# Optimization experiments

Hardware: AMD Instinct MI355X
Metric: run time of the kernel (lower is better)

The kernel has to match this reference:

```python
import jax, jax.numpy as jnp
import numpy as np

# ---- constants matching init_kwargs ----
N_GRID = 512
DX = 1.0 / N_GRID
INV_DX = float(N_GRID)
DT = 1e-4
P_VOL = (DX * 0.5) ** 2
P_RHO = 1.0
P_MASS = P_VOL * P_RHO
GRAVITY = 10.0
N_PART = 2_000_000


def setup_inputs() -> dict:
    key = jax.random.key(0)
    k = jax.random.split(key, 5)
    # positions safely inside the domain so the 3x3 stencil never leaves the grid
    x = 0.1 + 0.8 * jax.random.uniform(k[0], (N_PART, 2), dtype=jnp.float32)
    v = 0.1 * jax.random.normal(k[1], (N_PART, 2), dtype=jnp.float32)
    C = 0.5 * jax.random.normal(k[2], (N_PART, 2, 2), dtype=jnp.float32)
    # deformation gradient near identity -> det(F) > 0 (physical MPM state)
    F = jnp.eye(2, dtype=jnp.float32)[None] + 0.01 * jax.random.normal(k[3], (N_PART, 2, 2), dtype=jnp.float32)
    material = jax.random.randint(k[4], (N_PART,), 0, 3, dtype=jnp.int32)
    Jp = jnp.ones((N_PART,), dtype=jnp.float32)
    E = jnp.array([1000.0], dtype=jnp.float32)
    nu = jnp.array([0.2], dtype=jnp.float32)
    return {"x": x, "v": v, "C": C, "F": F, "material": material, "Jp": Jp, "E": E, "nu": nu}


def _quad_weights(fx):
    # quadratic B-spline weights; fx: (N,2), returns list of 3 arrays (N,2)
    return [0.5 * (1.5 - fx) ** 2, 0.75 - (fx - 1.0) ** 2, 0.5 * (fx - 0.5) ** 2]


def _polar_rotation_and_J(F):
    # Closed-form 2x2 polar decomposition F = R S. For det(F) > 0 this R equals
    # U @ Vh from the (embedded 3x3) SVD used by the torch code, and
    # J = prod(singular values) = |det F|.
    a = F[:, 0, 0] + F[:, 1, 1]
    b = F[:, 1, 0] - F[:, 0, 1]
    r = jnp.sqrt(a * a + b * b)
    c, s = a / r, b / r
    R = jnp.stack([jnp.stack([c, -s], -1), jnp.stack([s, c], -1)], -2)  # (N,2,2)
    J = jnp.abs(F[:, 0, 0] * F[:, 1, 1] - F[:, 0, 1] * F[:, 1, 0])
    return R, J


def _step(x, v, C, F, Jp, E, nu):
    mu0 = E / (2.0 * (1.0 + nu))                      # (1,)
    la0 = E * nu / ((1.0 + nu) * (1.0 - 2.0 * nu))    # (1,)

    base = (x * INV_DX - 0.5).astype(jnp.int32)       # (N,2)
    fx = x * INV_DX - base.astype(jnp.float32)        # (N,2)
    w = _quad_weights(fx)

    # deformation gradient update: F <- F + dt * C @ F
    F = F + DT * jnp.einsum('nij,njk->nik', C, F)

    h = jnp.exp(10.0 * (1.0 - Jp))                    # (N,)
    mu, la = mu0 * h, la0 * h                         # (N,)

    R, J = _polar_rotation_and_J(F)
    # 2*mu*(F - R) @ F^T + I * lambda*J*(J-1)
    PF = jnp.einsum('nij,nkj->nik', F - R, F)
    I2 = jnp.eye(2, dtype=F.dtype)
    stress = 2.0 * mu[:, None, None] * PF + I2[None] * (la * J * (J - 1.0))[:, None, None]
    stress = (-DT * P_VOL * 4.0 * INV_DX ** 2) * stress
    affine = stress + P_MASS * C                      # (N,2,2)

    # ---- P2G scatter: grid_v += w * (m*v + affine @ dpos), grid_m += w*m ----
    # (identical to the torch trick of scattering m*v - affine@x and affine,
    #  then adding scatter(affine) @ grid_x, since grid_x - x = (offset - fx)*dx)
    ncell = N_GRID * N_GRID
    grid_v = jnp.zeros((ncell, 2), dtype=F.dtype)
    grid_m = jnp.zeros((ncell,), dtype=F.dtype)
    mv = P_MASS * v
    for i in range(3):
        for j in range(3):
            off = jnp.array([i, j], dtype=fx.dtype)
            weight = w[i][:, 0] * w[j][:, 1]                      # (N,)
            dpos = (off - fx) * DX                                # (N,2)
            contrib = weight[:, None] * (mv + jnp.einsum('nij,nj->ni', affine, dpos))
            idx = (base[:, 0] + i) * N_GRID + (base[:, 1] + j)    # (N,)
            grid_v = grid_v.at[idx].add(contrib)
            grid_m = grid_m.at[idx].add(weight * P_MASS)
    grid_v = grid_v.reshape(N_GRID, N_GRID, 2)
    grid_m = grid_m.reshape(N_GRID, N_GRID)

    # momentum -> velocity only where mass > 0
    nonempty = grid_m > 0
    grid_v = jnp.where(nonempty[..., None], grid_v / jnp.maximum(grid_m, 1e-30)[..., None], grid_v)
    grid_v = grid_v.at[:, :, 1].add(-DT * GRAVITY)
    # boundary conditions
    grid_v = grid_v.at[:3, :, 0].set(jnp.maximum(grid_v[:3, :, 0], 0.0))
    grid_v = grid_v.at[-2:, :, 0].set(jnp.minimum(grid_v[-2:, :, 0], 0.0))
    grid_v = grid_v.at[:, :3, 1].set(jnp.maximum(grid_v[:, :3, 1], 0.0))
    grid_v = grid_v.at[:, -2:, 1].set(jnp.minimum(grid_v[:, -2:, 1], 0.0))

    # ---- G2P gather ----
    gv_flat = grid_v.reshape(ncell, 2)
    new_v = jnp.zeros_like(v)
    new_C = jnp.zeros_like(C)
    for i in range(3):
        for j in range(3):
            off = jnp.array([i, j], dtype=fx.dtype)
            weight = w[i][:, 0] * w[j][:, 1]
            dpos = (off - fx) * DX
            idx = (base[:, 0] + i) * N_GRID + (base[:, 1] + j)
            gv = gv_flat[idx]                                      # (N,2)
            new_v = new_v + weight[:, None] * gv
            new_C = new_C + (4.0 * INV_DX ** 2) * weight[:, None, None] * gv[:, :, None] * dpos[:, None, :]

    x = x + DT * new_v
    return x, new_v, new_C, F


def reference(x, v, C, F, material, Jp, E, nu):
    xn, vn, Cn, Fn = _step(x, v, C, F, Jp, E, nu)
    return (xn, vn, Cn, Fn, material, Jp)
```

## Files before the change

### kernel.cpp

```cpp
#include <hip/hip_runtime.h>

namespace {
constexpr int   NGRID  = 512;
constexpr int   NCELL  = NGRID * NGRID;
constexpr float DX     = 1.0f / (float)NGRID;
constexpr float INV_DX = (float)NGRID;
constexpr float DT     = 1e-4f;
constexpr float P_VOL  = (DX * 0.5f) * (DX * 0.5f);
constexpr float P_MASS = P_VOL * 1.0f;
constexpr float GRAV   = 10.0f;

constexpr int TILE  = 16;
constexpr int TPR   = NGRID / TILE;
constexpr int NTILE = TPR * TPR;
constexpr int REG   = TILE + 3;
constexpr int RCELL = REG * REG;
constexpr int NBLK  = 512;
constexpr int BLK   = 256;
constexpr int PBLK  = 512;
constexpr int CAP   = 3456;
constexpr int BINS  = 17 * 17;
}


__device__ __forceinline__ float quadw(int d, float fx) {
    const float t0 = 1.5f - fx, t1 = fx - 1.0f, t2 = fx - 0.5f;
    const float w0 = 0.5f * t0 * t0;
    const float w1 = 0.75f - t1 * t1;
    const float w2 = 0.5f * t2 * t2;
    return d == 0 ? w0 : (d == 1 ? w1 : w2);
}

__global__ __launch_bounds__(256) void k_count(
    const float2* __restrict__ x, int n, int ppb,
    int* __restrict__ cnt )
{
    __shared__ int hist[NTILE];
    for (int t = threadIdx.x; t < NTILE; t += BLK) hist[t] = 0;
    __syncthreads();
    const int b0 = blockIdx.x * ppb;
    const int b1 = min(b0 + ppb, n);
    for (int p = b0 + threadIdx.x; p < b1; p += BLK) {
        const float2 xp = x[p];
        const int ci = (int)(xp.x * INV_DX);
        const int cj = (int)(xp.y * INV_DX);
        atomicAdd(&hist[(ci >> 4) * TPR + (cj >> 4)], 1);
    }
    __syncthreads();
    int* row = cnt + (size_t)blockIdx.x * NTILE;
    for (int t = threadIdx.x; t < NTILE; t += BLK) row[t] = hist[t];
}

__global__ __launch_bounds__(1024) void k_scan(
    int* __restrict__ cnt, int* __restrict__ tile_start, int* __restrict__ tile_end)
{
    const int t = threadIdx.x;
    int s = 0;
    #pragma unroll 8
    for (int b = 0; b < NBLK; ++b) s += cnt[(size_t)b * NTILE + t];

    __shared__ int wsum[16];
    const int lane = t & 63, w = t >> 6;
    int inc = s;
    #pragma unroll
    for (int d = 1; d < 64; d <<= 1) {
        int u = __shfl_up(inc, d, 64);
        if (lane >= d) inc += u;
    }
    if (lane == 63) wsum[w] = inc;
    __syncthreads();
    if (t == 0) {
        int r = 0;
        #pragma unroll
        for (int i = 0; i < 16; ++i) { int v = wsum[i]; wsum[i] = r; r += v; }
    }
    __syncthreads();
    const int base = wsum[w] + inc - s;
    tile_start[t] = base;
    tile_end[t]   = base + s;

    int run = base;
    #pragma unroll 8
    for (int b = 0; b < NBLK; ++b) {
        int v = cnt[(size_t)b * NTILE + t];
        cnt[(size_t)b * NTILE + t] = run;
        run += v;
    }
}

__global__ __launch_bounds__(256) void k_scatter(
    const float2* __restrict__ x,
    const float2* __restrict__ v,
    const float4* __restrict__ C,
    const float4* __restrict__ F,
    const int*    __restrict__ material,
    const float*  __restrict__ Jp,
    const float*  __restrict__ Ep,
    const float*  __restrict__ nup,
    int n, int ppb,
    const int* __restrict__ cnt,
    float4* __restrict__ packed,
    float4* __restrict__ outF,
    float*  __restrict__ outMat,
    float*  __restrict__ outJp)
{
    __shared__ int cur[NTILE];
    {
        const int* row = cnt + (size_t)blockIdx.x * NTILE;
        for (int t = threadIdx.x; t < NTILE; t += BLK) cur[t] = row[t];
    }
    __syncthreads();

    const float E  = Ep[0];
    const float nu = nup[0];
    const float mu0 = E / (2.0f * (1.0f + nu));
    const float la0 = E * nu / ((1.0f + nu) * (1.0f - 2.0f * nu));

    const int b0 = blockIdx.x * ppb;
    const int b1 = min(b0 + ppb, n);
    for (int p = b0 + threadIdx.x; p < b1; p += BLK) {
        const float2 xp = x[p];
        const float2 vp = v[p];
        const float4 c4 = C[p];
        const float4 f4 = F[p];
        const float  jp = Jp[p];

        const float F00 = f4.x + DT * (c4.x * f4.x + c4.y * f4.z);
        const float F01 = f4.y + DT * (c4.x * f4.y + c4.y * f4.w);
        const float F10 = f4.z + DT * (c4.z * f4.x + c4.w * f4.z);
        const float F11 = f4.w + DT * (c4.z * f4.y + c4.w * f4.w);

        const float h  = expf(10.0f * (1.0f - jp));
        const float mu = mu0 * h;
        const float la = la0 * h;

        const float a = F00 + F11;
        const float b = F10 - F01;
        const float r = sqrtf(a * a + b * b);
        const float cth = a / r;
        const float sth = b / r;
        const float J = fabsf(F00 * F11 - F01 * F10);

        const float A00 = F00 - cth, A01 = F01 + sth;
        const float A10 = F10 - sth, A11 = F11 - cth;
        const float PF00 = A00 * F00 + A01 * F01;
        const float PF01 = A00 * F10 + A01 * F11;
        const float PF10 = A10 * F00 + A11 * F01;
        const float PF11 = A10 * F10 + A11 * F11;

        constexpr float SC = -DT * P_VOL * 4.0f * INV_DX * INV_DX;
        const float diag = la * J * (J - 1.0f);
        const float twomu = 2.0f * mu;
        const float Af00 = SC * (twomu * PF00 + diag) + P_MASS * c4.x;
        const float Af01 = SC * (twomu * PF01)        + P_MASS * c4.y;
        const float Af10 = SC * (twomu * PF10)        + P_MASS * c4.z;
        const float Af11 = SC * (twomu * PF11 + diag) + P_MASS * c4.w;

        const int ci = (int)(xp.x * INV_DX);
        const int cj = (int)(xp.y * INV_DX);
        const int t  = (ci >> 4) * TPR + (cj >> 4);
        const int slot = atomicAdd(&cur[t], 1);

        packed[2 * (size_t)slot]     = make_float4(xp.x, xp.y, P_MASS * vp.x, P_MASS * vp.y);
        packed[2 * (size_t)slot + 1] = make_float4(Af00, Af01, Af10, Af11);

        outF[p]   = make_float4(F00, F01, F10, F11);
        outMat[p] = (float)material[p];
        outJp[p]  = jp;
    }
}

__global__ __launch_bounds__(PBLK) void k_p2g_tile(
    const float4* __restrict__ packed,
    const int* __restrict__ tile_start,
    const int* __restrict__ tile_end,
    float* __restrict__ gvx, float* __restrict__ gvy, float* __restrict__ gm)
{
    const int t  = blockIdx.x;
    const int s0 = tile_start[t];
    const int s1 = tile_end[t];
    if (s0 == s1) return;

    __shared__ float4 rec[2 * CAP];
    __shared__ unsigned short perm[CAP];
    __shared__ unsigned short binof[CAP];
    __shared__ int bcnt[BINS];
    __shared__ int boffs[BINS];
    __shared__ int wscan[8];

    const int tid = threadIdx.x;
    const int tr = t >> 5, tc = t & 31;
    const int r0 = tr * TILE - 1, c0 = tc * TILE - 1;

    const int nseg = s1 - s0;
    const int nin  = min(nseg, CAP);
    const bool ovf = (nseg > CAP);

    for (int b = tid; b < BINS; b += PBLK) bcnt[b] = 0;
    __syncthreads();

    for (int k = tid; k < nin; k += PBLK) {
        const float4 pa = packed[2 * (size_t)(s0 + k)];
        const float4 pb = packed[2 * (size_t)(s0 + k) + 1];
        rec[2 * k]     = pa;
        rec[2 * k + 1] = pb;
        const int bi = (int)(pa.x * INV_DX - 0.5f);
        const int bj = (int)(pa.y * INV_DX - 0.5f);
        const int bin = (bi - r0) * 17 + (bj - c0);
        binof[k] = (unsigned short)bin;
        atomicAdd(&bcnt[bin], 1);
    }
    __syncthreads();

    int vv = 0, incl = 0;
    if (tid < 320) {
        vv = (tid < BINS) ? bcnt[tid] : 0;
        incl = vv;
        const int lane = tid & 63;
        #pragma unroll
        for (int d = 1; d < 64; d <<= 1) {
            int u = __shfl_up(incl, d, 64);
            if (lane >= d) incl += u;
        }
        if (lane == 63) wscan[tid >> 6] = incl;
    }
    __syncthreads();
    if (tid == 0) {
        int run = 0;
        #pragma unroll
        for (int i = 0; i < 5; ++i) { int w = wscan[i]; wscan[i] = run; run += w; }
    }
    __syncthreads();
    if (tid < BINS) {
        const int excl = incl - vv + wscan[tid >> 6];
        boffs[tid] = excl;
        bcnt[tid]  = excl;
    }
    __syncthreads();

    for (int k = tid; k < nin; k += PBLK) {
        const int bin = binof[k];
        const int rk = atomicAdd(&bcnt[bin], 1);
        perm[rk] = (unsigned short)k;
    }
    __syncthreads();

    if (ovf) {
        for (int k = CAP + tid; k < nseg; k += PBLK) {
            const float4 pa = packed[2 * (size_t)(s0 + k)];
            const float4 pb = packed[2 * (size_t)(s0 + k) + 1];
            const float xs = pa.x * INV_DX, ys = pa.y * INV_DX;
            const int bi = (int)(xs - 0.5f), bj = (int)(ys - 0.5f);
            const float fxx = xs - (float)bi, fxy = ys - (float)bj;
            for (int i = 0; i < 3; ++i)
                for (int j = 0; j < 3; ++j) {
                    const float wgt = quadw(i, fxx) * quadw(j, fxy);
                    const float dpx = ((float)i - fxx) * DX;
                    const float dpy = ((float)j - fxy) * DX;
                    const int g = (bi + i) * NGRID + (bj + j);
                    atomicAdd(&gvx[g], wgt * (pa.z + pb.x * dpx + pb.y * dpy));
                    atomicAdd(&gvy[g], wgt * (pa.w + pb.z * dpx + pb.w * dpy));
                    atomicAdd(&gm[g],  wgt * P_MASS);
                }
        }
    }

    for (int idx = tid; idx < RCELL; idx += PBLK) {
        const int lr = idx / REG, lc = idx % REG;
        float vx = 0.0f, vy = 0.0f, m = 0.0f;

        #pragma unroll
        for (int di = 0; di < 3; ++di) {
            const int bli = lr - di;
            if ((unsigned)bli > 16u) continue;
            #pragma unroll
            for (int dj = 0; dj < 3; ++dj) {
                const int blj = lc - dj;
                if ((unsigned)blj > 16u) continue;
                const int b = bli * 17 + blj;
                const int k0 = boffs[b], k1 = bcnt[b];
                for (int k = k0; k < k1; ++k) {
                    const int pp = perm[k];
                    const float4 pa = rec[2 * pp];
                    const float4 pb = rec[2 * pp + 1];
                    const float xs = pa.x * INV_DX, ys = pa.y * INV_DX;
                    const float fxx = xs - (float)((int)(xs - 0.5f));
                    const float fxy = ys - (float)((int)(ys - 0.5f));
                    const float wgt = quadw(di, fxx) * quadw(dj, fxy);
                    const float dpx = ((float)di - fxx) * DX;
                    const float dpy = ((float)dj - fxy) * DX;
                    vx += wgt * (pa.z + pb.x * dpx + pb.y * dpy);
                    vy += wgt * (pa.w + pb.z * dpx + pb.w * dpy);
                    m  += wgt * P_MASS;
                }
            }
        }

        const int gr = r0 + lr, gc = c0 + lc;
        if ((unsigned)gr >= (unsigned)NGRID || (unsigned)gc >= (unsigned)NGRID) continue;
        const int g = gr * NGRID + gc;
        const bool interior = (lr >= 3 && lr <= 15 && lc >= 3 && lc <= 15) && !ovf;
        if (interior) {
            gvx[g] = vx; gvy[g] = vy; gm[g] = m;
        } else {
            if (vx != 0.0f) atomicAdd(&gvx[g], vx);
            if (vy != 0.0f) atomicAdd(&gvy[g], vy);
            if (m  != 0.0f) atomicAdd(&gm[g],  m);
        }
    }
}

__global__ __launch_bounds__(256) void k_grid(
    const float* __restrict__ gvx, const float* __restrict__ gvy,
    const float* __restrict__ gm, float2* __restrict__ gv)
{
    const int idx = blockIdx.x * blockDim.x + threadIdx.x;
    if (idx >= NCELL) return;
    const int i = idx >> 9;
    const int j = idx & (NGRID - 1);
    float m = gm[idx], vx = gvx[idx], vy = gvy[idx];
    if (m > 0.0f) {
        const float inv = 1.0f / fmaxf(m, 1e-30f);
        vx *= inv; vy *= inv;
    }
    vy -= DT * GRAV;
    if (i < 3)          vx = fmaxf(vx, 0.0f);
    if (i >= NGRID - 2) vx = fminf(vx, 0.0f);
    if (j < 3)          vy = fmaxf(vy, 0.0f);
    if (j >= NGRID - 2) vy = fminf(vy, 0.0f);
    gv[idx] = make_float2(vx, vy);
}

__global__ __launch_bounds__(256) void k_g2p(
    const float2* __restrict__ x,
    const float2* __restrict__ gv,
    float2* __restrict__ outX,
    float2* __restrict__ outV,
    float4* __restrict__ outC,
    int n)
{
    const int p = blockIdx.x * blockDim.x + threadIdx.x;
    if (p >= n) return;

    const float2 xp = x[p];
    const float xs = xp.x * INV_DX, ys = xp.y * INV_DX;
    const int bi = (int)(xs - 0.5f);
    const int bj = (int)(ys - 0.5f);
    const float fxx = xs - (float)bi;
    const float fxy = ys - (float)bj;

    float wx[3], wy[3];
    { float t0 = 1.5f - fxx, t1 = fxx - 1.0f, t2 = fxx - 0.5f;
      wx[0] = 0.5f * t0 * t0; wx[1] = 0.75f - t1 * t1; wx[2] = 0.5f * t2 * t2; }
    { float t0 = 1.5f - fxy, t1 = fxy - 1.0f, t2 = fxy - 0.5f;
      wy[0] = 0.5f * t0 * t0; wy[1] = 0.75f - t1 * t1; wy[2] = 0.5f * t2 * t2; }

    float nvx = 0.0f, nvy = 0.0f;
    float C00 = 0.0f, C01 = 0.0f, C10 = 0.0f, C11 = 0.0f;
    constexpr float K4 = 4.0f * INV_DX * INV_DX;

    #pragma unroll
    for (int i = 0; i < 3; ++i) {
        const float dpx = ((float)i - fxx) * DX;
        const int rowbase = (bi + i) * NGRID + bj;
        #pragma unroll
        for (int j = 0; j < 3; ++j) {
            const float wgt = wx[i] * wy[j];
            const float dpy = ((float)j - fxy) * DX;
            const float2 g = gv[rowbase + j];
            nvx += wgt * g.x;
            nvy += wgt * g.y;
            const float kw = K4 * wgt;
            C00 += kw * g.x * dpx;
            C01 += kw * g.x * dpy;
            C10 += kw * g.y * dpx;
            C11 += kw * g.y * dpy;
        }
    }

    outX[p] = make_float2(xp.x + DT * nvx, xp.y + DT * nvy);
    outV[p] = make_float2(nvx, nvy);
    outC[p] = make_float4(C00, C01, C10, C11);
}

__global__ __launch_bounds__(256) void fb_p2g(
    const float2* __restrict__ x, const float2* __restrict__ v,
    const float4* __restrict__ C, const float4* __restrict__ F,
    const int* __restrict__ material, const float* __restrict__ Jp,
    const float* __restrict__ Ep, const float* __restrict__ nup,
    float* __restrict__ g,
    float4* __restrict__ outF, float* __restrict__ outMat, float* __restrict__ outJp,
    int n)
{
    const int p = blockIdx.x * blockDim.x + threadIdx.x;
    if (p >= n) return;
    const float E = Ep[0], nu = nup[0];
    const float mu0 = E / (2.0f * (1.0f + nu));
    const float la0 = E * nu / ((1.0f + nu) * (1.0f - 2.0f * nu));
    const float2 xp = x[p]; const float2 vp = v[p];
    const float4 c4 = C[p]; const float4 f4 = F[p];
    const float jp = Jp[p];
    const float xs = xp.x * INV_DX, ys = xp.y * INV_DX;
    const int bi = (int)(xs - 0.5f), bj = (int)(ys - 0.5f);
    const float fxx = xs - (float)bi, fxy = ys - (float)bj;
    float wx[3], wy[3];
    { float t0 = 1.5f - fxx, t1 = fxx - 1.0f, t2 = fxx - 0.5f;
      wx[0] = 0.5f * t0 * t0; wx[1] = 0.75f - t1 * t1; wx[2] = 0.5f * t2 * t2; }
    { float t0 = 1.5f - fxy, t1 = fxy - 1.0f, t2 = fxy - 0.5f;
      wy[0] = 0.5f * t0 * t0; wy[1] = 0.75f - t1 * t1; wy[2] = 0.5f * t2 * t2; }
    const float F00 = f4.x + DT * (c4.x * f4.x + c4.y * f4.z);
    const float F01 = f4.y + DT * (c4.x * f4.y + c4.y * f4.w);
    const float F10 = f4.z + DT * (c4.z * f4.x + c4.w * f4.z);
    const float F11 = f4.w + DT * (c4.z * f4.y + c4.w * f4.w);
    const float h = expf(10.0f * (1.0f - jp));
    const float mu = mu0 * h, la = la0 * h;
    const float a = F00 + F11, b = F10 - F01;
    const float r = sqrtf(a * a + b * b);
    const float cth = a / r, sth = b / r;
    const float J = fabsf(F00 * F11 - F01 * F10);
    const float A00 = F00 - cth, A01 = F01 + sth;
    const float A10 = F10 - sth, A11 = F11 - cth;
    constexpr float SC = -DT * P_VOL * 4.0f * INV_DX * INV_DX;
    const float diag = la * J * (J - 1.0f);
    const float twomu = 2.0f * mu;
    const float Af00 = SC * (twomu * (A00 * F00 + A01 * F01) + diag) + P_MASS * c4.x;
    const float Af01 = SC * (twomu * (A00 * F10 + A01 * F11))        + P_MASS * c4.y;
    const float Af10 = SC * (twomu * (A10 * F00 + A11 * F01))        + P_MASS * c4.z;
    const float Af11 = SC * (twomu * (A10 * F10 + A11 * F11) + diag) + P_MASS * c4.w;
    const float mvx = P_MASS * vp.x, mvy = P_MASS * vp.y;
    #pragma unroll
    for (int i = 0; i < 3; ++i) {
        #pragma unroll
        for (int j = 0; j < 3; ++j) {
            const float wgt = wx[i] * wy[j];
            const float dpx = ((float)i - fxx) * DX;
            const float dpy = ((float)j - fxy) * DX;
            const size_t k3 = (size_t)((bi + i) * NGRID + (bj + j)) * 3;
            atomicAdd(&g[k3 + 0], wgt * (mvx + Af00 * dpx + Af01 * dpy));
            atomicAdd(&g[k3 + 1], wgt * (mvy + Af10 * dpx + Af11 * dpy));
            atomicAdd(&g[k3 + 2], wgt * P_MASS);
        }
    }
    outF[p] = make_float4(F00, F01, F10, F11);
    outMat[p] = (float)material[p];
    outJp[p] = jp;
}

__global__ __launch_bounds__(256) void fb_grid(
    const float* __restrict__ g, float2* __restrict__ gv)
{
    const int idx = blockIdx.x * blockDim.x + threadIdx.x;
    if (idx >= NCELL) return;
    const int i = idx >> 9, j = idx & (NGRID - 1);
    float vx = g[(size_t)idx * 3], vy = g[(size_t)idx * 3 + 1], m = g[(size_t)idx * 3 + 2];
    if (m > 0.0f) { const float inv = 1.0f / fmaxf(m, 1e-30f); vx *= inv; vy *= inv; }
    vy -= DT * GRAV;
    if (i < 3)          vx = fmaxf(vx, 0.0f);
    if (i >= NGRID - 2) vx = fminf(vx, 0.0f);
    if (j < 3)          vy = fmaxf(vy, 0.0f);
    if (j >= NGRID - 2) vy = fminf(vy, 0.0f);
    gv[idx] = make_float2(vx, vy);
}

extern "C" void kernel_launch(void* const* d_in, const int* in_sizes, int n_in,
                              void* d_out, int out_size, void* d_ws, size_t ws_size,
                              hipStream_t stream) {
    const int n = in_sizes[0] / 2;

    const float2* x   = (const float2*)d_in[0];
    const float2* v   = (const float2*)d_in[1];
    const float4* C   = (const float4*)d_in[2];
    const float4* F   = (const float4*)d_in[3];
    const int*    mat = (const int*)d_in[4];
    const float*  Jp  = (const float*)d_in[5];
    const float*  Ep  = (const float*)d_in[6];
    const float*  nup = (const float*)d_in[7];

    float* out = (float*)d_out;
    float2* o_x = (float2*)(out);
    float2* o_v = (float2*)(out + 2 * (size_t)n);
    float4* o_C = (float4*)(out + 4 * (size_t)n);
    float4* o_F = (float4*)(out + 8 * (size_t)n);
    float*  o_m = out + 12 * (size_t)n;
    float*  o_J = out + 13 * (size_t)n;

    const int BLOCK = 256;
    const int pgrid = (n + BLOCK - 1) / BLOCK;
    const int ggrid = (NCELL + BLOCK - 1) / BLOCK;

    char* w = (char*)d_ws;
    float4* packed = (float4*)w;            w += (size_t)n * 2 * sizeof(float4);
    int* cnt    = (int*)w;                  w += (size_t)NBLK * NTILE * sizeof(int);
    int* tstart = (int*)w;                  w += (size_t)NTILE * sizeof(int);
    int* tend   = (int*)w;                  w += (size_t)NTILE * sizeof(int);
    float* gvx  = (float*)w;                w += (size_t)NCELL * sizeof(float);
    float* gvy  = (float*)w;                w += (size_t)NCELL * sizeof(float);
    float* gm   = (float*)w;                w += (size_t)NCELL * sizeof(float);
    float2* gfin= (float2*)w;               w += (size_t)NCELL * sizeof(float2);
    const size_t need = (size_t)(w - (char*)d_ws);

    if (ws_size >= need) {
        const int ppb = (n + NBLK - 1) / NBLK;
        hipMemsetAsync(gvx, 0, (size_t)NCELL * 3 * sizeof(float), stream);
        k_count  <<<NBLK, BLOCK, 0, stream>>>(x, n, ppb, cnt);
        k_scan   <<<1, 1024, 0, stream>>>(cnt, tstart, tend);
        k_scatter<<<NBLK, BLOCK, 0, stream>>>(x, v, C, F, mat, Jp, Ep, nup,
                                              n, ppb, cnt, packed, o_F, o_m, o_J);
        k_p2g_tile<<<NTILE, PBLK, 0, stream>>>(packed, tstart, tend, gvx, gvy, gm);
        k_grid   <<<ggrid, BLOCK, 0, stream>>>(gvx, gvy, gm, gfin);
        k_g2p    <<<pgrid, BLOCK, 0, stream>>>(x, gfin, o_x, o_v, o_C, n);
    } else {
        float* g = (float*)d_ws;
        float2* gf = (float2*)(g + (size_t)NCELL * 3);
        hipMemsetAsync(g, 0, (size_t)NCELL * 3 * sizeof(float), stream);
        fb_p2g <<<pgrid, BLOCK, 0, stream>>>(x, v, C, F, mat, Jp, Ep, nup,
                                             g, o_F, o_m, o_J, n);
        fb_grid<<<ggrid, BLOCK, 0, stream>>>(g, gf);
        k_g2p  <<<pgrid, BLOCK, 0, stream>>>(x, gf, o_x, o_v, o_C, n);
    }
}
```

Baseline: 497.2 us.

## Drop shared particle staging in P2G tile kernel and merge bin-row loops

The tile P2G kernel no longer copies particle records into a large shared-memory buffer. It only reads positions to bin them, then the gather loop reads the packed particle data straight from global memory, relying on the cache. The three per-column bin loops are merged into one contiguous range per bin row, and the column offset is computed per particle. Block size drops from 512 to 384 threads. Freeing about 110KB of LDS should allow more blocks per CU, but every cell now issues repeated global or L2 loads in place of LDS reads.

Result: slower. 566.7 us (+14.0%).

```diff
diff --git a/kernel.cpp b/kernel.cpp
--- a/kernel.cpp
+++ b/kernel.cpp
@@ -17,7 +17,7 @@
 constexpr int RCELL = REG * REG;
 constexpr int NBLK  = 512;
 constexpr int BLK   = 256;
-constexpr int PBLK  = 512;
+constexpr int PBLK  = 384;
 constexpr int CAP   = 3456;
 constexpr int BINS  = 17 * 17;
 }
@@ -181,7 +181,6 @@
     const int s1 = tile_end[t];
     if (s0 == s1) return;
 
-    __shared__ float4 rec[2 * CAP];
     __shared__ unsigned short perm[CAP];
     __shared__ unsigned short binof[CAP];
     __shared__ int bcnt[BINS];
@@ -200,12 +199,9 @@
     __syncthreads();
 
     for (int k = tid; k < nin; k += PBLK) {
-        const float4 pa = packed[2 * (size_t)(s0 + k)];
-        const float4 pb = packed[2 * (size_t)(s0 + k) + 1];
-        rec[2 * k]     = pa;
-        rec[2 * k + 1] = pb;
-        const int bi = (int)(pa.x * INV_DX - 0.5f);
-        const int bj = (int)(pa.y * INV_DX - 0.5f);
+        const float2 xy = *(const float2*)&packed[2 * (size_t)(s0 + k)];
+        const int bi = (int)(xy.x * INV_DX - 0.5f);
+        const int bj = (int)(xy.y * INV_DX - 0.5f);
         const int bin = (bi - r0) * 17 + (bj - c0);
         binof[k] = (unsigned short)bin;
         atomicAdd(&bcnt[bin], 1);
@@ -269,30 +265,31 @@
         const int lr = idx / REG, lc = idx % REG;
         float vx = 0.0f, vy = 0.0f, m = 0.0f;
 
+        const int blj_lo = max(lc - 2, 0), blj_hi = min(lc, 16);
+
         #pragma unroll
         for (int di = 0; di < 3; ++di) {
             const int bli = lr - di;
             if ((unsigned)bli > 16u) continue;
-            #pragma unroll
-            for (int dj = 0; dj < 3; ++dj) {
-                const int blj = lc - dj;
-                if ((unsigned)blj > 16u) continue;
-                const int b = bli * 17 + blj;
-                const int k0 = boffs[b], k1 = bcnt[b];
-                for (int k = k0; k < k1; ++k) {
-                    const int pp = perm[k];
-                    const float4 pa = rec[2 * pp];
-                    const float4 pb = rec[2 * pp + 1];
-                    const float xs = pa.x * INV_DX, ys = pa.y * INV_DX;
-                    const float fxx = xs - (float)((int)(xs - 0.5f));
-                    const float fxy = ys - (float)((int)(ys - 0.5f));
-                    const float wgt = quadw(di, fxx) * quadw(dj, fxy);
-                    const float dpx = ((float)di - fxx) * DX;
-                    const float dpy = ((float)dj - fxy) * DX;
-                    vx += wgt * (pa.z + pb.x * dpx + pb.y * dpy);
-                    vy += wgt * (pa.w + pb.z * dpx + pb.w * dpy);
-                    m  += wgt * P_MASS;
-                }
+            const int  brow = bli * 17;
+            const int  k0 = boffs[brow + blj_lo];
+            const int  k1 = bcnt[brow + blj_hi];
+            for (int k = k0; k < k1; ++k) {
+                const int pp = perm[k];
+                const float4 pa = packed[2 * (size_t)(s0 + pp)];
+                const float4 pb = packed[2 * (size_t)(s0 + pp) + 1];
+                const float xs = pa.x * INV_DX, ys = pa.y * INV_DX;
+                const int  bi = (int)(xs - 0.5f);
+                const int  bj = (int)(ys - 0.5f);
+                const float fxx = xs - (float)bi;
+                const float fxy = ys - (float)bj;
+                const int  dj = lc - (bj - c0);
+                const float wgt = quadw(di, fxx) * quadw(dj, fxy);
+                const float dpx = ((float)di - fxx) * DX;
+                const float dpy = ((float)dj - fxy) * DX;
+                vx += wgt * (pa.z + pb.x * dpx + pb.y * dpy);
+                vy += wgt * (pa.w + pb.z * dpx + pb.w * dpy);
+                m  += wgt * P_MASS;
             }
         }
 
```
